# Optimization experiments

Hardware: AMD Instinct MI355X
Metric: run time of the kernel (lower is better)

Reference implementation:

```python
import jax, jax.numpy as jnp
import numpy as np

BETA = 0.95      # config.snn_beta
THR = 1.0        # snntorch Leaky default threshold
SLOPE = 10.0     # config.surrogate_slope (fast_sigmoid)
T = 16           # config.snn_timesteps
A_PLUS, A_MINUS = 0.008, 0.01
ELIG_DECAY = 0.95

# Heaviside spike with fast-sigmoid surrogate gradient: d/dm = 1/(slope*|m-thr|+1)^2
@jax.custom_vjp
def spike_fn(m):
    return (m > THR).astype(m.dtype)

def _spk_fwd(m):
    return spike_fn(m), m

def _spk_bwd(m, g):
    return (g / (SLOPE * jnp.abs(m - THR) + 1.0) ** 2,)

spike_fn.defvjp(_spk_fwd, _spk_bwd)


def setup_inputs() -> dict:
    key = jax.random.key(0)
    ks = jax.random.split(key, 7)
    B, S, H, A = 65536, 25, 64, 4

    def lin_w(k, o, i):
        lim = 1.0 / np.sqrt(i)
        return jax.random.uniform(k, (o, i), jnp.float32, -lim, lim)

    def lin_b(k, o, i):
        lim = 1.0 / np.sqrt(i)
        return jax.random.uniform(k, (o,), jnp.float32, -lim, lim)

    return {
        "x": jax.random.normal(ks[0], (B, S), jnp.float32),
        "W1": lin_w(ks[1], H, S), "b1": lin_b(ks[2], H, S),
        "W2": lin_w(ks[3], H, H), "b2": lin_b(ks[4], H, H),
        "W3": lin_w(ks[5], A, H), "b3": lin_b(ks[6], A, H),
        "elig0": jnp.zeros((A, H), jnp.float32),  # eligibility trace (fc3.out, fc3.in)
    }


def reference(x, W1, b1, W2, b2, W3, b3, elig0):
    B = x.shape[0]
    H = W1.shape[0]
    A = W3.shape[0]
    cur1 = x @ W1.T + b1  # input current is identical every timestep

    def step(carry, _):
        m1, m2, m3, elig, acc = carry
        m1 = BETA * m1 + cur1
        s1 = spike_fn(m1)
        m1 = m1 - s1 * THR
        m2 = BETA * m2 + s1 @ W2.T + b2
        s2 = spike_fn(m2)
        m2 = m2 - s2 * THR
        m3 = BETA * m3 + s2 @ W3.T + b3
        s3 = spike_fn(m3)
        m3 = m3 - s3 * THR
        pre = jax.lax.stop_gradient(s2).mean(0)   # [H]
        post = jax.lax.stop_gradient(s3).mean(0)  # [A]
        elig = ELIG_DECAY * elig + (A_PLUS - A_MINUS) * jnp.outer(post, pre)
        return (m1, m2, m3, elig, acc + s3), None

    init = (
        jnp.zeros((B, H), x.dtype),
        jnp.zeros((B, H), x.dtype),
        jnp.zeros((B, A), x.dtype),
        elig0,
        jnp.zeros((B, A), x.dtype),
    )
    (_, _, _, elig, acc), _ = jax.lax.scan(step, init, None, length=T)
    readout = acc / T  # mean over timesteps of spk3
    probs = jax.nn.softmax(readout, axis=-1)
    return probs, elig
```

## Files before the change

### kernel.cpp

```cpp
#include <hip/hip_runtime.h>

#define T_STEPS 16
#define H 64
#define S_IN 25
#define A_OUT 4
#define NB 65536
#define UPW 8
#define WPB 8
#define EPB 128

typedef unsigned long long ull;

__device__ __forceinline__ float fmaf_(float a, float b, float c) { return __builtin_fmaf(a, b, c); }

__global__ void snn_prep(const float* __restrict__ W2, const float* __restrict__ W3,
                         float* __restrict__ W2T, float* __restrict__ W3T) {
    int i = blockIdx.x * blockDim.x + threadIdx.x;
    if (i < H * H) { int h = i >> 6, k = i & 63; W2T[k * H + h] = W2[h * H + k]; }
    if (i < A_OUT * H) { int a = i >> 6, h = i & 63; W3T[h * A_OUT + a] = W3[a * H + h]; }
}

__global__ __launch_bounds__(512, 4) void snn_main(
    const float* __restrict__ x,
    const float* __restrict__ W1, const float* __restrict__ b1,
    const float* __restrict__ W2T, const float* __restrict__ b2,
    const float* __restrict__ W3T, const float* __restrict__ b3,
    float* __restrict__ out, int* __restrict__ g_pre, int* __restrict__ g_post)
{
#pragma clang fp contract(off)
    __shared__ unsigned char s1bits[T_STEPS][EPB][8];
    __shared__ float4 w3s[H];
    __shared__ unsigned int s2buf[2][WPB][EPB];
    __shared__ float m3acc[EPB][8];
    __shared__ int lds_pre[T_STEPS * H];
    __shared__ int lds_post[T_STEPS * A_OUT];

    const int tid = threadIdx.x;
    if (tid < H) w3s[tid] = reinterpret_cast<const float4*>(W3T)[tid];
    for (int i = tid; i < T_STEPS * H; i += 512) lds_pre[i] = 0;
    if (tid < T_STEPS * A_OUT) lds_post[tid] = 0;
    for (int i = tid; i < EPB * 8; i += 512) (&m3acc[0][0])[i] = 0.0f;

    const int lane  = tid & 63;
    const int wq    = __builtin_amdgcn_readfirstlane(tid >> 6);
    const int hbase = UPW * wq;
    const int bA    = blockIdx.x * EPB + lane;
    const int bB    = bA + 64;

    {
        float cur1A[UPW], cur1B[UPW];
        float xv[S_IN];
        #pragma unroll
        for (int s = 0; s < S_IN; ++s) xv[s] = x[bA * S_IN + s];
        #pragma unroll
        for (int j = 0; j < UPW; ++j) {
            int h = hbase + j;
            float acc = 0.0f;
            #pragma unroll
            for (int s = 0; s < S_IN; ++s) acc = fmaf_(xv[s], W1[h * S_IN + s], acc);
            cur1A[j] = acc + b1[h];
        }
        #pragma unroll
        for (int s = 0; s < S_IN; ++s) xv[s] = x[bB * S_IN + s];
        #pragma unroll
        for (int j = 0; j < UPW; ++j) {
            int h = hbase + j;
            float acc = 0.0f;
            #pragma unroll
            for (int s = 0; s < S_IN; ++s) acc = fmaf_(xv[s], W1[h * S_IN + s], acc);
            cur1B[j] = acc + b1[h];
        }

        float m1A[UPW], m1B[UPW];
        #pragma unroll
        for (int j = 0; j < UPW; ++j) { m1A[j] = 0.0f; m1B[j] = 0.0f; }
        for (int t = 0; t < T_STEPS; ++t) {
            unsigned int sA = 0u, sB = 0u;
            #pragma unroll
            for (int j = 0; j < UPW; ++j) {
                float ma = 0.95f * m1A[j]; ma = ma + cur1A[j];
                bool pa = ma > 1.0f; m1A[j] = pa ? (ma - 1.0f) : ma; sA |= (pa ? 1u : 0u) << j;
                float mb = 0.95f * m1B[j]; mb = mb + cur1B[j];
                bool pb = mb > 1.0f; m1B[j] = pb ? (mb - 1.0f) : mb; sB |= (pb ? 1u : 0u) << j;
            }
            s1bits[t][lane][wq]      = (unsigned char)sA;
            s1bits[t][lane + 64][wq] = (unsigned char)sB;
        }
    }

    float m2A[UPW], m2B[UPW];
    #pragma unroll
    for (int j = 0; j < UPW; ++j) { m2A[j] = 0.0f; m2B[j] = 0.0f; }

    __syncthreads();

    for (int t = 0; t < T_STEPS; ++t) {
        const int slot = t & 1;

        const ull mA = *reinterpret_cast<const ull*>(&s1bits[t][lane][0]);
        const ull mB = *reinterpret_cast<const ull*>(&s1bits[t][lane + 64][0]);
        const unsigned int mloA = (unsigned int)mA, mhiA = (unsigned int)(mA >> 32);
        const unsigned int mloB = (unsigned int)mB, mhiB = (unsigned int)(mB >> 32);

        #pragma unroll
        for (int j = 0; j < UPW; ++j) { m2A[j] = 0.95f * m2A[j]; m2B[j] = 0.95f * m2B[j]; }

        #pragma unroll 8
        for (int k = 0; k < 32; ++k) {
            const float sfA = (float)((mloA >> k) & 1u);
            const float sfB = (float)((mloB >> k) & 1u);
            const float* wr = W2T + k * H + hbase;
            #pragma unroll
            for (int j = 0; j < UPW; ++j) {
                const float w = wr[j];
                m2A[j] = fmaf_(sfA, w, m2A[j]);
                m2B[j] = fmaf_(sfB, w, m2B[j]);
            }
        }
        #pragma unroll 8
        for (int k = 0; k < 32; ++k) {
            const float sfA = (float)((mhiA >> k) & 1u);
            const float sfB = (float)((mhiB >> k) & 1u);
            const float* wr = W2T + (k + 32) * H + hbase;
            #pragma unroll
            for (int j = 0; j < UPW; ++j) {
                const float w = wr[j];
                m2A[j] = fmaf_(sfA, w, m2A[j]);
                m2B[j] = fmaf_(sfB, w, m2B[j]);
            }
        }

        unsigned int s2A = 0u, s2B = 0u;
        int myCnt = 0;
        #pragma unroll
        for (int j = 0; j < UPW; ++j) {
            float ma = m2A[j] + b2[hbase + j];
            bool pa = ma > 1.0f;
            m2A[j] = ma - (pa ? 1.0f : 0.0f);
            s2A |= (pa ? 1u : 0u) << j;
            float mb = m2B[j] + b2[hbase + j];
            bool pb = mb > 1.0f;
            m2B[j] = mb - (pb ? 1.0f : 0.0f);
            s2B |= (pb ? 1u : 0u) << j;
            int cnt = (int)__popcll(__ballot(pa)) + (int)__popcll(__ballot(pb));
            myCnt = (lane == j) ? cnt : myCnt;
        }
        s2buf[slot][wq][lane] = s2A;
        s2buf[slot][wq][lane + 64] = s2B;
        if (lane < UPW) lds_pre[t * H + hbase + lane] = myCnt;

        __syncthreads();

        const int duty = wq & 3;
        if (duty == (t & 3)) {
            const int el = (wq < 4) ? lane : (lane + 64);
            unsigned int q0 = s2buf[slot][0][el], q1 = s2buf[slot][1][el];
            unsigned int q2 = s2buf[slot][2][el], q3 = s2buf[slot][3][el];
            unsigned int q4 = s2buf[slot][4][el], q5 = s2buf[slot][5][el];
            unsigned int q6 = s2buf[slot][6][el], q7 = s2buf[slot][7][el];
            ull s2v = (ull)(q0 | (q1 << 8) | (q2 << 16) | (q3 << 24))
                    | ((ull)(q4 | (q5 << 8) | (q6 << 16) | (q7 << 24)) << 32);
            float m3[A_OUT], ac[A_OUT];
            #pragma unroll
            for (int a = 0; a < A_OUT; ++a) { m3[a] = 0.95f * m3acc[el][a]; ac[a] = m3acc[el][4 + a]; }
            for (int h = 0; h < H; ++h) {
                float s2f = (float)((unsigned)s2v & 1u);
                s2v >>= 1;
                const float4 w = w3s[h];
                m3[0] = fmaf_(s2f, w.x, m3[0]);
                m3[1] = fmaf_(s2f, w.y, m3[1]);
                m3[2] = fmaf_(s2f, w.z, m3[2]);
                m3[3] = fmaf_(s2f, w.w, m3[3]);
            }
            int myPost = 0;
            #pragma unroll
            for (int a = 0; a < A_OUT; ++a) {
                float m = m3[a] + b3[a];
                bool sp = m > 1.0f;
                float s3f = sp ? 1.0f : 0.0f;
                m3[a] = m - s3f;
                ac[a] = ac[a] + s3f;
                int c = (int)__popcll(__ballot(sp));
                myPost = (lane == a) ? c : myPost;
            }
            if (lane < A_OUT) atomicAdd(&lds_post[t * A_OUT + lane], myPost);
            if (t == T_STEPS - 1) {
                float r0 = ac[0] * 0.0625f, r1 = ac[1] * 0.0625f;
                float r2 = ac[2] * 0.0625f, r3 = ac[3] * 0.0625f;
                float mx = fmaxf(fmaxf(r0, r1), fmaxf(r2, r3));
                float e0 = expf(r0 - mx), e1 = expf(r1 - mx);
                float e2 = expf(r2 - mx), e3 = expf(r3 - mx);
                float s = ((e0 + e1) + e2) + e3;
                reinterpret_cast<float4*>(out)[blockIdx.x * EPB + el] =
                    make_float4(e0 / s, e1 / s, e2 / s, e3 / s);
            } else {
                #pragma unroll
                for (int a = 0; a < A_OUT; ++a) { m3acc[el][a] = m3[a]; m3acc[el][4 + a] = ac[a]; }
            }
        }
    }

    __syncthreads();
    for (int i = tid; i < T_STEPS * H; i += 512) atomicAdd(&g_pre[i], lds_pre[i]);
    if (tid < T_STEPS * A_OUT) atomicAdd(&g_post[tid], lds_post[tid]);
}

__global__ void snn_elig(const int* __restrict__ g_pre, const int* __restrict__ g_post,
                         const float* __restrict__ elig0, float* __restrict__ out) {
#pragma clang fp contract(off)
    int i = threadIdx.x;
    int a = i >> 6, h = i & 63;
    float e = elig0[i];
    const float invB = 1.0f / 65536.0f;
    for (int t = 0; t < T_STEPS; ++t) {
        float pre  = (float)g_pre[t * H + h] * invB;
        float post = (float)g_post[t * A_OUT + a] * invB;
        e = 0.95f * e + (-0.002f) * (post * pre);
    }
    out[NB * A_OUT + i] = e;
}

extern "C" void kernel_launch(void* const* d_in, const int* in_sizes, int n_in,
                              void* d_out, int out_size, void* d_ws, size_t ws_size,
                              hipStream_t stream) {
    const float* x     = (const float*)d_in[0];
    const float* W1    = (const float*)d_in[1];
    const float* b1    = (const float*)d_in[2];
    const float* W2    = (const float*)d_in[3];
    const float* b2    = (const float*)d_in[4];
    const float* W3    = (const float*)d_in[5];
    const float* b3    = (const float*)d_in[6];
    const float* elig0 = (const float*)d_in[7];
    float* out = (float*)d_out;

    char* ws = (char*)d_ws;
    int*   g_pre  = (int*)(ws);
    int*   g_post = (int*)(ws + 4096);
    float* W2T    = (float*)(ws + 8192);
    float* W3T    = (float*)(ws + 8192 + 16384);

    (void)hipMemsetAsync(ws, 0, 4096 + 256, stream);
    snn_prep<<<17, 256, 0, stream>>>(W2, W3, W2T, W3T);
    snn_main<<<NB / EPB, 512, 0, stream>>>(x, W1, b1, W2T, b2, W3T, b3, out, g_pre, g_post);
    snn_elig<<<1, 256, 0, stream>>>(g_pre, g_post, elig0, out);
}
```

Baseline: 166.7 us.

## Stage layer-1 spikes as double-buffered float LDS tiles instead of packed bits

Layer-1 spikes are now kept in registers as 64-bit masks per thread. Each step they are expanded into a double-buffered float array in LDS laid out [h][element], so the layer-2 inner loop reads spike values directly instead of extracting and converting bits. This removes the per-k shift, mask and int-to-float work. In exchange each k iteration issues two extra LDS reads, each step adds LDS writes of the next timestep's spikes, and LDS footprint grows, which may cut occupancy.

```diff
diff --git a/kernel.cpp b/kernel.cpp
--- a/kernel.cpp
+++ b/kernel.cpp
@@ -28,7 +28,7 @@
     float* __restrict__ out, int* __restrict__ g_pre, int* __restrict__ g_post)
 {
 #pragma clang fp contract(off)
-    __shared__ unsigned char s1bits[T_STEPS][EPB][8];
+    __shared__ float s1f[2][H][EPB];
     __shared__ float4 w3s[H];
     __shared__ unsigned int s2buf[2][WPB][EPB];
     __shared__ float m3acc[EPB][8];
@@ -47,6 +47,7 @@
     const int bA    = blockIdx.x * EPB + lane;
     const int bB    = bA + 64;
 
+    ull mskA0 = 0ull, mskA1 = 0ull, mskB0 = 0ull, mskB1 = 0ull;
     {
         float cur1A[UPW], cur1B[UPW];
         float xv[S_IN];
@@ -74,7 +75,7 @@
         float m1A[UPW], m1B[UPW];
         #pragma unroll
         for (int j = 0; j < UPW; ++j) { m1A[j] = 0.0f; m1B[j] = 0.0f; }
-        for (int t = 0; t < T_STEPS; ++t) {
+        for (int t = 0; t < 8; ++t) {
             unsigned int sA = 0u, sB = 0u;
             #pragma unroll
             for (int j = 0; j < UPW; ++j) {
@@ -83,9 +84,33 @@
                 float mb = 0.95f * m1B[j]; mb = mb + cur1B[j];
                 bool pb = mb > 1.0f; m1B[j] = pb ? (mb - 1.0f) : mb; sB |= (pb ? 1u : 0u) << j;
             }
-            s1bits[t][lane][wq]      = (unsigned char)sA;
-            s1bits[t][lane + 64][wq] = (unsigned char)sB;
-        }
+            mskA0 |= ((ull)sA) << (8 * t);
+            mskB0 |= ((ull)sB) << (8 * t);
+        }
+        for (int t = 0; t < 8; ++t) {
+            unsigned int sA = 0u, sB = 0u;
+            #pragma unroll
+            for (int j = 0; j < UPW; ++j) {
+                float ma = 0.95f * m1A[j]; ma = ma + cur1A[j];
+                bool pa = ma > 1.0f; m1A[j] = pa ? (ma - 1.0f) : ma; sA |= (pa ? 1u : 0u) << j;
+                float mb = 0.95f * m1B[j]; mb = mb + cur1B[j];
+                bool pb = mb > 1.0f; m1B[j] = pb ? (mb - 1.0f) : mb; sB |= (pb ? 1u : 0u) << j;
+            }
+            mskA1 |= ((ull)sA) << (8 * t);
+            mskB1 |= ((ull)sB) << (8 * t);
+        }
+    }
+
+    {
+        unsigned int uA = (unsigned int)mskA0 & 0xFFu;
+        unsigned int uB = (unsigned int)mskB0 & 0xFFu;
+        #pragma unroll
+        for (int j = 0; j < UPW; ++j) {
+            s1f[0][hbase + j][lane]      = ((uA >> j) & 1u) ? 1.0f : 0.0f;
+            s1f[0][hbase + j][lane + 64] = ((uB >> j) & 1u) ? 1.0f : 0.0f;
+        }
+        mskA0 = (mskA0 >> 8) | (mskA1 << 56); mskA1 >>= 8;
+        mskB0 = (mskB0 >> 8) | (mskB1 << 56); mskB1 >>= 8;
     }
 
     float m2A[UPW], m2B[UPW];
@@ -97,31 +122,14 @@
     for (int t = 0; t < T_STEPS; ++t) {
         const int slot = t & 1;
 
-        const ull mA = *reinterpret_cast<const ull*>(&s1bits[t][lane][0]);
-        const ull mB = *reinterpret_cast<const ull*>(&s1bits[t][lane + 64][0]);
-        const unsigned int mloA = (unsigned int)mA, mhiA = (unsigned int)(mA >> 32);
-        const unsigned int mloB = (unsigned int)mB, mhiB = (unsigned int)(mB >> 32);
-
         #pragma unroll
         for (int j = 0; j < UPW; ++j) { m2A[j] = 0.95f * m2A[j]; m2B[j] = 0.95f * m2B[j]; }
 
         #pragma unroll 8
-        for (int k = 0; k < 32; ++k) {
-            const float sfA = (float)((mloA >> k) & 1u);
-            const float sfB = (float)((mloB >> k) & 1u);
+        for (int k = 0; k < H; ++k) {
+            const float sfA = s1f[slot][k][lane];
+            const float sfB = s1f[slot][k][lane + 64];
             const float* wr = W2T + k * H + hbase;
-            #pragma unroll
-            for (int j = 0; j < UPW; ++j) {
-                const float w = wr[j];
-                m2A[j] = fmaf_(sfA, w, m2A[j]);
-                m2B[j] = fmaf_(sfB, w, m2B[j]);
-            }
-        }
-        #pragma unroll 8
-        for (int k = 0; k < 32; ++k) {
-            const float sfA = (float)((mhiA >> k) & 1u);
-            const float sfB = (float)((mhiB >> k) & 1u);
-            const float* wr = W2T + (k + 32) * H + hbase;
             #pragma unroll
             for (int j = 0; j < UPW; ++j) {
                 const float w = wr[j];
@@ -148,6 +156,18 @@
         s2buf[slot][wq][lane] = s2A;
         s2buf[slot][wq][lane + 64] = s2B;
         if (lane < UPW) lds_pre[t * H + hbase + lane] = myCnt;
+
+        if (t < T_STEPS - 1) {
+            unsigned int uA = (unsigned int)mskA0 & 0xFFu;
+            unsigned int uB = (unsigned int)mskB0 & 0xFFu;
+            #pragma unroll
+            for (int j = 0; j < UPW; ++j) {
+                s1f[slot ^ 1][hbase + j][lane]      = ((uA >> j) & 1u) ? 1.0f : 0.0f;
+                s1f[slot ^ 1][hbase + j][lane + 64] = ((uB >> j) & 1u) ? 1.0f : 0.0f;
+            }
+            mskA0 = (mskA0 >> 8) | (mskA1 << 56); mskA1 >>= 8;
+            mskB0 = (mskB0 >> 8) | (mskB1 << 56); mskB1 >>= 8;
+        }
 
         __syncthreads();
 
```

Measured after the change: 227.1 us. 36.2% more time.
